# Kernel tuning notes

Hardware: AMD Instinct MI355X
Metric: run time of the kernel (lower is better)

The kernel has to match this reference:

```python
import jax, jax.numpy as jnp
import numpy as np

B, S, D = 2, 2048, 2048
NH, NKV = 16, 4
HD = D // NH          # 128
Q_DIM = NH * HD       # 2048
KV_DIM = NKV * HD     # 512
N_REP = NH // NKV     # 4


def setup_inputs() -> dict:
    key = jax.random.key(0)
    k1, k2, k3, k4 = jax.random.split(key, 4)
    x = jax.random.normal(k1, (B, S, D), dtype=jnp.float32)
    freqs_cis = jax.random.normal(k2, (S, HD), dtype=jnp.float32)
    Wqkv = jax.random.normal(k3, (Q_DIM + 2 * KV_DIM, D), dtype=jnp.float32) * (D ** -0.5)
    Wo = jax.random.normal(k4, (D, Q_DIM), dtype=jnp.float32) * (Q_DIM ** -0.5)
    return {"x": x, "freqs_cis": freqs_cis, "Wqkv": Wqkv, "Wo": Wo}


def _apply_rope(xq, xk, freqs_cis):
    # xq: [B,S,NH,HD], xk: [B,S,NKV,HD], freqs_cis: [S,HD] viewed as [S,1,HD//2,2]
    f = freqs_cis.reshape(S, 1, HD // 2, 2)
    f0, f1 = f[..., 0], f[..., 1]  # broadcast over batch & heads

    def rot(t):
        shp = t.shape
        tp = t.reshape(*shp[:-1], HD // 2, 2)
        t0, t1 = tp[..., 0], tp[..., 1]
        # row1 = <x, (f0,f1)>;  row0 = <x, (f1,-f0)>  (matches torch flip+negate)
        row1 = t0 * f0 + t1 * f1
        row0 = t0 * f1 - t1 * f0
        return jnp.stack([row0, row1], axis=-1).reshape(shp)

    return rot(xq), rot(xk)


def reference(x, freqs_cis, Wqkv, Wo):
    # Fused QKV projection (exact path: all RLA sketch dims = 0)
    xqkv = jnp.einsum('bsd,od->bso', x, Wqkv)
    xq = xqkv[..., :Q_DIM].reshape(B, S, NH, HD)
    xk = xqkv[..., Q_DIM:Q_DIM + KV_DIM].reshape(B, S, NKV, HD)
    xv = xqkv[..., Q_DIM + KV_DIM:].reshape(B, S, NKV, HD)

    xq, xk = _apply_rope(xq, xk, freqs_cis)

    # [B,H,S,HD]
    xq = xq.transpose(0, 2, 1, 3)
    xk = xk.transpose(0, 2, 1, 3)
    xv = xv.transpose(0, 2, 1, 3)

    # GQA: repeat kv heads n_rep times
    xk = jnp.repeat(xk, N_REP, axis=1)
    xv = jnp.repeat(xv, N_REP, axis=1)

    scale = 1.0 / jnp.sqrt(jnp.asarray(HD, dtype=xq.dtype))
    scores = jnp.einsum('bhqd,bhkd->bhqk', xq, xk) * scale
    causal = jnp.tril(jnp.ones((S, S), dtype=bool))
    scores = jnp.where(causal, scores, jnp.finfo(scores.dtype).min)
    probs = jax.nn.softmax(scores, axis=-1)
    out = jnp.einsum('bhqk,bhkd->bhqd', probs, xv)  # [B,H,S,HD]

    out = out.transpose(0, 2, 1, 3).reshape(B, S, Q_DIM)
    return jnp.einsum('bsq,dq->bsd', out, Wo)
```

## Files before the change

kernel.cpp:

```cpp
#include <hip/hip_runtime.h>
#include <hip/hip_bf16.h>
#include <cstdint>
#include <cstddef>

#define B_ 2
#define S_ 2048
#define NH_ 16
#define NKV_ 4
#define HD_ 128
#define QDIM_ 2048
#define KVDIM_ 512
#define QKV_ 3072

typedef __attribute__((ext_vector_type(8))) short short8;
typedef __attribute__((ext_vector_type(4))) short bhalf4;
typedef __attribute__((ext_vector_type(4))) float float4v;

__device__ __forceinline__ float bf2f(short u) {
  union { unsigned int i; float f; } v;
  v.i = ((unsigned int)(unsigned short)u) << 16;
  return v.f;
}
__device__ __forceinline__ short f2bf(float f) {
  union { float f; unsigned int i; } v; v.f = f;
  unsigned int x = v.i;
  x += 0x7fffu + ((x >> 16) & 1u);
  return (short)(x >> 16);
}

#if __has_builtin(__builtin_amdgcn_exp2f)
__device__ __forceinline__ float exp2fast(float x) { return __builtin_amdgcn_exp2f(x); }
#else
__device__ __forceinline__ float exp2fast(float x) { return exp2f(x); }
#endif

__device__ __forceinline__ unsigned int cvt_pk_bf16(float a, float b) {
  unsigned int r;
  asm("v_cvt_pk_bf16_f32 %0, %1, %2" : "=v"(r) : "v"(a), "v"(b));
  return r;
}

__device__ __forceinline__ void async_copy16(void* lds, const void* g) {
  __builtin_amdgcn_global_load_lds(
      (const __attribute__((address_space(1))) void*)g,
      (__attribute__((address_space(3))) void*)lds, 16, 0, 0);
}

__device__ __forceinline__ void cvt8(const float* f, short* d) {
  float4v a = *(const float4v*)(f);
  float4v b = *(const float4v*)(f + 4);
  short8 r;
#pragma unroll
  for (int e = 0; e < 4; ++e) { r[e] = f2bf(a[e]); r[4 + e] = f2bf(b[e]); }
  *(short8*)d = r;
}

__global__ void f32_to_bf16(const float* __restrict__ src, short* __restrict__ dst,
                            int n8) {
  int id = blockIdx.x * 256 + threadIdx.x;
  if (id >= n8) return;
  cvt8(src + (size_t)id * 8, dst + (size_t)id * 8);
}

__global__ void f32_to_bf16_2(const float* __restrict__ s0, short* __restrict__ d0,
                              int n0_8, const float* __restrict__ s1,
                              short* __restrict__ d1) {
  int id = blockIdx.x * 256 + threadIdx.x;
  if (id < n0_8) {
    cvt8(s0 + (size_t)id * 8, d0 + (size_t)id * 8);
  } else {
    int j = id - n0_8;
    cvt8(s1 + (size_t)j * 8, d1 + (size_t)j * 8);
  }
}

template <int N, int K, bool CF32>
__global__ __launch_bounds__(256)
void gemm_nt_bf16(const short* __restrict__ A, const short* __restrict__ Bm,
                  void* __restrict__ Cp) {
  __shared__ __align__(16) short sA[128 * 32];
  __shared__ __align__(16) short sB[128 * 32];
  const int tid = threadIdx.x;
  const int m0 = blockIdx.y * 128, n0 = blockIdx.x * 128;
  const int wave = tid >> 6, lane = tid & 63;
  const int wm = (wave & 1) << 6, wn = (wave >> 1) << 6;
  const int lm = lane & 15, kg = lane >> 4;

  float4v acc[4][4];
#pragma unroll
  for (int i = 0; i < 4; ++i)
#pragma unroll
    for (int j = 0; j < 4; ++j)
      acc[i][j] = (float4v){0.f, 0.f, 0.f, 0.f};

  const int r0 = tid >> 2, c0 = tid & 3;
  const short* gA0 = A + (size_t)(m0 + r0) * K + c0 * 8;
  const short* gA1 = gA0 + (size_t)64 * K;
  const short* gB0 = Bm + (size_t)(n0 + r0) * K + c0 * 8;
  const short* gB1 = gB0 + (size_t)64 * K;
  short* lA0 = sA + tid * 8;
  short* lA1 = sA + 2048 + tid * 8;
  short* lB0 = sB + tid * 8;
  short* lB1 = sB + 2048 + tid * 8;

  for (int k0 = 0; k0 < K; k0 += 32) {
    async_copy16(lA0, gA0 + k0);
    async_copy16(lA1, gA1 + k0);
    async_copy16(lB0, gB0 + k0);
    async_copy16(lB1, gB1 + k0);
    __syncthreads();

    short8 a[4], b[4];
#pragma unroll
    for (int i = 0; i < 4; ++i)
      a[i] = *(const short8*)(sA + (wm + i * 16 + lm) * 32 + kg * 8);
#pragma unroll
    for (int j = 0; j < 4; ++j)
      b[j] = *(const short8*)(sB + (wn + j * 16 + lm) * 32 + kg * 8);
#pragma unroll
    for (int i = 0; i < 4; ++i)
#pragma unroll
      for (int j = 0; j < 4; ++j)
        acc[i][j] = __builtin_amdgcn_mfma_f32_16x16x32_bf16(a[i], b[j], acc[i][j], 0, 0, 0);
    __syncthreads();
  }

#pragma unroll
  for (int i = 0; i < 4; ++i) {
    const int rb = m0 + wm + i * 16 + kg * 4;
#pragma unroll
    for (int j = 0; j < 4; ++j) {
      const int cc = n0 + wn + j * 16 + lm;
#pragma unroll
      for (int r = 0; r < 4; ++r) {
        if constexpr (CF32)
          ((float*)Cp)[(size_t)(rb + r) * N + cc] = acc[i][j][r];
        else
          ((short*)Cp)[(size_t)(rb + r) * N + cc] = f2bf(acc[i][j][r]);
      }
    }
  }
}

__global__ void rope_split(const short* __restrict__ xqkv, const float* __restrict__ freqs,
                           short* __restrict__ Qr, short* __restrict__ Kr,
                           short* __restrict__ Vv) {
  const int id = blockIdx.x * 256 + threadIdx.x;
  const int i = id / (QKV_ / 8);
  const int c8 = id % (QKV_ / 8);
  const int col = c8 * 8;
  const int b = i >> 11, s = i & (S_ - 1);
  short8 xv = *(const short8*)(xqkv + (size_t)i * QKV_ + col);
  if (col < QDIM_ + KVDIM_) {
    int d;
    short* dst;
    float sc;
    if (col < QDIM_) {
      int hh = col >> 7; d = col & 127;
      dst = Qr + ((size_t)(b * NH_ + hh) * S_ + s) * HD_ + d;
      sc = 0.12751744543795287f;
    } else {
      int cc = col - QDIM_;
      int hh = cc >> 7; d = cc & 127;
      dst = Kr + ((size_t)(b * NKV_ + hh) * S_ + s) * HD_ + d;
      sc = 1.0f;
    }
    const float* fp = freqs + (size_t)s * HD_ + d;
    float4v fa = *(const float4v*)(fp);
    float4v fb = *(const float4v*)(fp + 4);
    float ff[8] = {fa[0], fa[1], fa[2], fa[3], fb[0], fb[1], fb[2], fb[3]};
    short8 ov;
#pragma unroll
    for (int pp = 0; pp < 4; ++pp) {
      float t0 = bf2f(xv[2 * pp]), t1 = bf2f(xv[2 * pp + 1]);
      float f0 = ff[2 * pp], f1 = ff[2 * pp + 1];
      ov[2 * pp]     = f2bf((t0 * f1 - t1 * f0) * sc);
      ov[2 * pp + 1] = f2bf((t0 * f0 + t1 * f1) * sc);
    }
    *(short8*)dst = ov;
  } else {
    int cc = col - QDIM_ - KVDIM_;
    int hh = cc >> 7, d = cc & 127;
    *(short8*)(Vv + ((size_t)(b * NKV_ + hh) * S_ + s) * HD_ + d) = xv;
  }
}

__global__ void transpose_v(const short* __restrict__ Vv, short* __restrict__ Vt) {
  __shared__ short t[64][72];
  const int s0 = blockIdx.x * 64, d0 = blockIdx.y * 64;
  const short* src = Vv + (size_t)blockIdx.z * S_ * HD_;
  short* dst = Vt + (size_t)blockIdx.z * S_ * HD_;
  const int tid = threadIdx.x;
#pragma unroll
  for (int c = 0; c < 2; ++c) {
    int ch = tid + 256 * c;
    int row = ch >> 3, kc = ch & 7;
    *(short8*)(&t[row][kc * 8]) =
        *(const short8*)(src + (size_t)(s0 + row) * HD_ + d0 + kc * 8);
  }
  __syncthreads();
#pragma unroll
  for (int c = 0; c < 2; ++c) {
    int ch = tid + 256 * c;
    int drow = ch >> 3, sc = ch & 7;
    short8 w;
#pragma unroll
    for (int j = 0; j < 8; ++j) w[j] = t[sc * 8 + j][drow];
    *(short8*)(dst + (size_t)(d0 + drow) * S_ + s0 + sc * 8) = w;
  }
}

#define TK 128

__global__ __launch_bounds__(256, 2)
void attn_causal(const short* __restrict__ Q, const short* __restrict__ K,
                 const short* __restrict__ Vt, short* __restrict__ O) {
  const int bh = blockIdx.x;
  const int qt = 31 - (int)blockIdx.y;
  const int b = bh >> 4, h = bh & 15;
  const int kvh = h >> 2;
  const int tid = threadIdx.x, wave = tid >> 6, lane = tid & 63;
  const int lm = lane & 15, kg = lane >> 4;

  __shared__ __align__(16) short sK[TK * HD_];
  __shared__ __align__(16) short sVt[HD_ * TK];

  const short* Qb = Q + (size_t)(b * NH_ + h) * S_ * HD_;
  const short* Kb = K + (size_t)(b * NKV_ + kvh) * S_ * HD_;
  const short* Vtb = Vt + (size_t)(b * NKV_ + kvh) * S_ * HD_;

  auto stageK = [&](int k0) {
#pragma unroll
    for (int c = 0; c < 8; ++c) {
      int ch = tid + 256 * c;
      int row = ch >> 4, kc = ch & 15;
      async_copy16(sK + ch * 8,
                   Kb + (size_t)(k0 + row) * HD_ + (kc ^ (row & 7)) * 8);
    }
  };
  auto stageV = [&](int k0) {
#pragma unroll
    for (int c = 0; c < 8; ++c) {
      int ch = tid + 256 * c;
      int row = ch >> 4, kc = ch & 15;
      async_copy16(sVt + ch * 8,
                   Vtb + (size_t)row * S_ + k0 + (kc ^ (row & 7)) * 8);
    }
  };

  const int qglob = qt * 64 + wave * 16 + lm;
  short8 qf[4];
#pragma unroll
  for (int kk = 0; kk < 4; ++kk)
    qf[kk] = *(const short8*)(Qb + (size_t)qglob * HD_ + kk * 32 + kg * 8);

  float mcur = -1e9f, lcur = 0.f;
  float4v o[8];
#pragma unroll
  for (int df = 0; df < 8; ++df) o[df] = (float4v){0.f, 0.f, 0.f, 0.f};

  stageK(0);
  const int nst = (qt + 2) >> 1;
  for (int s = 0; s < nst; ++s) {
    const int k0 = s * TK;
    const bool last = (s == nst - 1);

    __syncthreads();
    stageV(k0);

    float4v sfT[8];
#pragma unroll
    for (int mj = 0; mj < 8; ++mj) sfT[mj] = (float4v){0.f, 0.f, 0.f, 0.f};
    __builtin_amdgcn_s_setprio(1);
#pragma unroll
    for (int kk = 0; kk < 4; ++kk) {
      int kd = kk * 4 + kg;
#pragma unroll
      for (int mj = 0; mj < 8; ++mj) {
        int row = mj * 16 + lm;
        short8 af = *(const short8*)(sK + row * HD_ + (kd ^ (row & 7)) * 8);
        sfT[mj] = __builtin_amdgcn_mfma_f32_16x16x32_bf16(af, qf[kk], sfT[mj], 0, 0, 0);
      }
    }
    __builtin_amdgcn_s_setprio(0);

    if (last) {
#pragma unroll
      for (int mj = 0; mj < 8; ++mj)
#pragma unroll
        for (int r = 0; r < 4; ++r) {
          int kcol = k0 + mj * 16 + kg * 4 + r;
          sfT[mj][r] = (kcol <= qglob) ? sfT[mj][r] : -3e38f;
        }
    }

    float mx = -3e38f;
#pragma unroll
    for (int mj = 0; mj < 8; ++mj)
#pragma unroll
      for (int r = 0; r < 4; ++r) mx = fmaxf(mx, sfT[mj][r]);
    mx = fmaxf(mx, __shfl_xor(mx, 16, 64));
    mx = fmaxf(mx, __shfl_xor(mx, 32, 64));
    const bool need = (mx > mcur + 4.f);
    const float mnew = fmaxf(mcur, mx);
    const float alpha = need ? exp2fast(mcur - mnew) : 1.f;
    const float m_use = need ? mnew : mcur;
    float rs = 0.f;
    bhalf4 pb[8];
#pragma unroll
    for (int t = 0; t < 8; ++t) {
      float e0 = exp2fast(sfT[t][0] - m_use);
      float e1 = exp2fast(sfT[t][1] - m_use);
      float e2 = exp2fast(sfT[t][2] - m_use);
      float e3 = exp2fast(sfT[t][3] - m_use);
      rs += (e0 + e1) + (e2 + e3);
      union { unsigned int u[2]; bhalf4 v; } pk;
      pk.u[0] = cvt_pk_bf16(e0, e1);
      pk.u[1] = cvt_pk_bf16(e2, e3);
      pb[t] = pk.v;
    }
    rs += __shfl_xor(rs, 16, 64);
    rs += __shfl_xor(rs, 32, 64);
    mcur = m_use;
    lcur = lcur * alpha + rs;

    __syncthreads();
    if (!last) stageK(k0 + TK);

    if (__any(need)) {
#pragma unroll
      for (int df = 0; df < 8; ++df)
#pragma unroll
        for (int r = 0; r < 4; ++r) o[df][r] *= alpha;
    }

    __builtin_amdgcn_s_setprio(1);
#pragma unroll
    for (int t = 0; t < 8; ++t) {
      int kc = t * 2 + (kg >> 1);
#pragma unroll
      for (int df = 0; df < 8; ++df) {
        int row = df * 16 + lm;
        bhalf4 va = *(const bhalf4*)(sVt + row * TK + (kc ^ (row & 7)) * 8 +
                                     (kg & 1) * 4);
        o[df] = __builtin_amdgcn_mfma_f32_16x16x16bf16_1k(va, pb[t], o[df], 0, 0, 0);
      }
    }
    __builtin_amdgcn_s_setprio(0);
  }

  const float inv = 1.f / lcur;
  const size_t rowoff = (size_t)(b * S_ + qglob) * QDIM_ + h * HD_ + kg * 4;
#pragma unroll
  for (int df = 0; df < 8; ++df) {
    bhalf4 w;
    w[0] = f2bf(o[df][0] * inv);
    w[1] = f2bf(o[df][1] * inv);
    w[2] = f2bf(o[df][2] * inv);
    w[3] = f2bf(o[df][3] * inv);
    *(bhalf4*)(O + rowoff + df * 16) = w;
  }
}

extern "C" void kernel_launch(void* const* d_in, const int* in_sizes, int n_in,
                              void* d_out, int out_size, void* d_ws, size_t ws_size,
                              hipStream_t stream) {
  const float* x     = (const float*)d_in[0];
  const float* freqs = (const float*)d_in[1];
  const float* Wqkv  = (const float*)d_in[2];
  const float* Wo    = (const float*)d_in[3];
  float* out = (float*)d_out;

  short* ws     = (short*)d_ws;
  short* xb     = ws;
  short* Wob    = ws;
  short* Wqkvb  = ws + (size_t)4096 * 2048;
  short* xqkv   = Wqkvb + (size_t)QKV_ * 2048;
  short* attn   = xqkv;
  short* Qr     = xqkv + (size_t)4096 * QKV_;
  short* Kr     = Qr + (size_t)B_ * NH_ * S_ * HD_;
  short* Vv     = Kr + (size_t)B_ * NKV_ * S_ * HD_;
  short* Vtg    = Vv + (size_t)B_ * NKV_ * S_ * HD_;

  f32_to_bf16_2<<<(4096 * 2048 / 8 + QKV_ * 2048 / 8) / 256, 256, 0, stream>>>(
      x, xb, 4096 * 2048 / 8, Wqkv, Wqkvb);
  gemm_nt_bf16<QKV_, 2048, false>
      <<<dim3(QKV_ / 128, 4096 / 128), 256, 0, stream>>>(xb, Wqkvb, xqkv);
  f32_to_bf16<<<(2048 * 2048 / 8) / 256, 256, 0, stream>>>(Wo, Wob, 2048 * 2048 / 8);
  rope_split<<<(B_ * S_ * QKV_ / 8) / 256, 256, 0, stream>>>(xqkv, freqs, Qr, Kr, Vv);
  transpose_v<<<dim3(S_ / 64, HD_ / 64, B_ * NKV_), 256, 0, stream>>>(Vv, Vtg);
  attn_causal<<<dim3(32, 32), 256, 0, stream>>>(Qr, Kr, Vtg, attn);
  gemm_nt_bf16<2048, 2048, true>
      <<<dim3(2048 / 128, 4096 / 128), 256, 0, stream>>>(attn, Wob, out);
}
```

Baseline: 309.6 us.

## Process 128 query rows per attention block to reuse K/V tiles

```diff
diff --git a/kernel.cpp b/kernel.cpp
--- a/kernel.cpp
+++ b/kernel.cpp
@@ -216,7 +216,8 @@
 void attn_causal(const short* __restrict__ Q, const short* __restrict__ K,
                  const short* __restrict__ Vt, short* __restrict__ O) {
   const int bh = blockIdx.x;
-  const int qt = 31 - (int)blockIdx.y;
+  const int by = blockIdx.y;
+  const int qt = (by < 8) ? (15 - by) : (by - 8);
   const int b = bh >> 4, h = bh & 15;
   const int kvh = h >> 2;
   const int tid = threadIdx.x, wave = tid >> 6, lane = tid & 63;
@@ -248,19 +249,24 @@
     }
   };
 
-  const int qglob = qt * 64 + wave * 16 + lm;
-  short8 qf[4];
-#pragma unroll
-  for (int kk = 0; kk < 4; ++kk)
-    qf[kk] = *(const short8*)(Qb + (size_t)qglob * HD_ + kk * 32 + kg * 8);
-
-  float mcur = -1e9f, lcur = 0.f;
-  float4v o[8];
-#pragma unroll
-  for (int df = 0; df < 8; ++df) o[df] = (float4v){0.f, 0.f, 0.f, 0.f};
+  const int qbase = qt * 128 + wave * 32 + lm;
+  short8 qf[2][4];
+#pragma unroll
+  for (int u = 0; u < 2; ++u)
+#pragma unroll
+    for (int kk = 0; kk < 4; ++kk)
+      qf[u][kk] = *(const short8*)(Qb + (size_t)(qbase + u * 16) * HD_ +
+                                   kk * 32 + kg * 8);
+
+  float mcur[2] = {-1e9f, -1e9f}, lcur[2] = {0.f, 0.f};
+  float4v o[2][8];
+#pragma unroll
+  for (int u = 0; u < 2; ++u)
+#pragma unroll
+    for (int df = 0; df < 8; ++df) o[u][df] = (float4v){0.f, 0.f, 0.f, 0.f};
 
   stageK(0);
-  const int nst = (qt + 2) >> 1;
+  const int nst = qt + 1;
   for (int s = 0; s < nst; ++s) {
     const int k0 = s * TK;
     const bool last = (s == nst - 1);
@@ -268,9 +274,11 @@
     __syncthreads();
     stageV(k0);
 
-    float4v sfT[8];
-#pragma unroll
-    for (int mj = 0; mj < 8; ++mj) sfT[mj] = (float4v){0.f, 0.f, 0.f, 0.f};
+    float4v sf[2][8];
+#pragma unroll
+    for (int u = 0; u < 2; ++u)
+#pragma unroll
+      for (int mj = 0; mj < 8; ++mj) sf[u][mj] = (float4v){0.f, 0.f, 0.f, 0.f};
     __builtin_amdgcn_s_setprio(1);
 #pragma unroll
     for (int kk = 0; kk < 4; ++kk) {
@@ -279,59 +287,72 @@
       for (int mj = 0; mj < 8; ++mj) {
         int row = mj * 16 + lm;
         short8 af = *(const short8*)(sK + row * HD_ + (kd ^ (row & 7)) * 8);
-        sfT[mj] = __builtin_amdgcn_mfma_f32_16x16x32_bf16(af, qf[kk], sfT[mj], 0, 0, 0);
+        sf[0][mj] = __builtin_amdgcn_mfma_f32_16x16x32_bf16(af, qf[0][kk], sf[0][mj], 0, 0, 0);
+        sf[1][mj] = __builtin_amdgcn_mfma_f32_16x16x32_bf16(af, qf[1][kk], sf[1][mj], 0, 0, 0);
       }
     }
     __builtin_amdgcn_s_setprio(0);
 
     if (last) {
 #pragma unroll
+      for (int u = 0; u < 2; ++u) {
+        const int qg = qbase + u * 16;
+#pragma unroll
+        for (int mj = 0; mj < 8; ++mj)
+#pragma unroll
+          for (int r = 0; r < 4; ++r) {
+            int kcol = k0 + mj * 16 + kg * 4 + r;
+            sf[u][mj][r] = (kcol <= qg) ? sf[u][mj][r] : -3e38f;
+          }
+      }
+    }
+
+    bhalf4 pb[2][8];
+    bool need[2];
+    float alpha[2];
+#pragma unroll
+    for (int u = 0; u < 2; ++u) {
+      float mx = -3e38f;
+#pragma unroll
       for (int mj = 0; mj < 8; ++mj)
 #pragma unroll
-        for (int r = 0; r < 4; ++r) {
-          int kcol = k0 + mj * 16 + kg * 4 + r;
-          sfT[mj][r] = (kcol <= qglob) ? sfT[mj][r] : -3e38f;
-        }
-    }
-
-    float mx = -3e38f;
-#pragma unroll
-    for (int mj = 0; mj < 8; ++mj)
-#pragma unroll
-      for (int r = 0; r < 4; ++r) mx = fmaxf(mx, sfT[mj][r]);
-    mx = fmaxf(mx, __shfl_xor(mx, 16, 64));
-    mx = fmaxf(mx, __shfl_xor(mx, 32, 64));
-    const bool need = (mx > mcur + 4.f);
-    const float mnew = fmaxf(mcur, mx);
-    const float alpha = need ? exp2fast(mcur - mnew) : 1.f;
-    const float m_use = need ? mnew : mcur;
-    float rs = 0.f;
-    bhalf4 pb[8];
-#pragma unroll
-    for (int t = 0; t < 8; ++t) {
-      float e0 = exp2fast(sfT[t][0] - m_use);
-      float e1 = exp2fast(sfT[t][1] - m_use);
-      float e2 = exp2fast(sfT[t][2] - m_use);
-      float e3 = exp2fast(sfT[t][3] - m_use);
-      rs += (e0 + e1) + (e2 + e3);
-      union { unsigned int u[2]; bhalf4 v; } pk;
-      pk.u[0] = cvt_pk_bf16(e0, e1);
-      pk.u[1] = cvt_pk_bf16(e2, e3);
-      pb[t] = pk.v;
-    }
-    rs += __shfl_xor(rs, 16, 64);
-    rs += __shfl_xor(rs, 32, 64);
-    mcur = m_use;
-    lcur = lcur * alpha + rs;
+        for (int r = 0; r < 4; ++r) mx = fmaxf(mx, sf[u][mj][r]);
+      mx = fmaxf(mx, __shfl_xor(mx, 16, 64));
+      mx = fmaxf(mx, __shfl_xor(mx, 32, 64));
+      need[u] = (mx > mcur[u] + 4.f);
+      const float mnew = fmaxf(mcur[u], mx);
+      alpha[u] = need[u] ? exp2fast(mcur[u] - mnew) : 1.f;
+      const float m_use = need[u] ? mnew : mcur[u];
+      float rs = 0.f;
+#pragma unroll
+      for (int t = 0; t < 8; ++t) {
+        float e0 = exp2fast(sf[u][t][0] - m_use);
+        float e1 = exp2fast(sf[u][t][1] - m_use);
+        float e2 = exp2fast(sf[u][t][2] - m_use);
+        float e3 = exp2fast(sf[u][t][3] - m_use);
+        rs += (e0 + e1) + (e2 + e3);
+        union { unsigned int w[2]; bhalf4 v; } pk;
+        pk.w[0] = cvt_pk_bf16(e0, e1);
+        pk.w[1] = cvt_pk_bf16(e2, e3);
+        pb[u][t] = pk.v;
+      }
+      rs += __shfl_xor(rs, 16, 64);
+      rs += __shfl_xor(rs, 32, 64);
+      mcur[u] = m_use;
+      lcur[u] = lcur[u] * alpha[u] + rs;
+    }
 
     __syncthreads();
     if (!last) stageK(k0 + TK);
 
-    if (__any(need)) {
-#pragma unroll
-      for (int df = 0; df < 8; ++df)
-#pragma unroll
-        for (int r = 0; r < 4; ++r) o[df][r] *= alpha;
+#pragma unroll
+    for (int u = 0; u < 2; ++u) {
+      if (__any(need[u])) {
+#pragma unroll
+        for (int df = 0; df < 8; ++df)
+#pragma unroll
+          for (int r = 0; r < 4; ++r) o[u][df][r] *= alpha[u];
+      }
     }
 
     __builtin_amdgcn_s_setprio(1);
@@ -343,22 +364,27 @@
         int row = df * 16 + lm;
         bhalf4 va = *(const bhalf4*)(sVt + row * TK + (kc ^ (row & 7)) * 8 +
                                      (kg & 1) * 4);
-        o[df] = __builtin_amdgcn_mfma_f32_16x16x16bf16_1k(va, pb[t], o[df], 0, 0, 0);
+        o[0][df] = __builtin_amdgcn_mfma_f32_16x16x16bf16_1k(va, pb[0][t], o[0][df], 0, 0, 0);
+        o[1][df] = __builtin_amdgcn_mfma_f32_16x16x16bf16_1k(va, pb[1][t], o[1][df], 0, 0, 0);
       }
     }
     __builtin_amdgcn_s_setprio(0);
   }
 
-  const float inv = 1.f / lcur;
-  const size_t rowoff = (size_t)(b * S_ + qglob) * QDIM_ + h * HD_ + kg * 4;
-#pragma unroll
-  for (int df = 0; df < 8; ++df) {
-    bhalf4 w;
-    w[0] = f2bf(o[df][0] * inv);
-    w[1] = f2bf(o[df][1] * inv);
-    w[2] = f2bf(o[df][2] * inv);
-    w[3] = f2bf(o[df][3] * inv);
-    *(bhalf4*)(O + rowoff + df * 16) = w;
+#pragma unroll
+  for (int u = 0; u < 2; ++u) {
+    const float inv = 1.f / lcur[u];
+    const size_t rowoff =
+        (size_t)(b * S_ + qbase + u * 16) * QDIM_ + h * HD_ + kg * 4;
+#pragma unroll
+    for (int df = 0; df < 8; ++df) {
+      bhalf4 w;
+      w[0] = f2bf(o[u][df][0] * inv);
+      w[1] = f2bf(o[u][df][1] * inv);
+      w[2] = f2bf(o[u][df][2] * inv);
+      w[3] = f2bf(o[u][df][3] * inv);
+      *(bhalf4*)(O + rowoff + df * 16) = w;
+    }
   }
 }
 
@@ -389,7 +415,7 @@
   f32_to_bf16<<<(2048 * 2048 / 8) / 256, 256, 0, stream>>>(Wo, Wob, 2048 * 2048 / 8);
   rope_split<<<(B_ * S_ * QKV_ / 8) / 256, 256, 0, stream>>>(xqkv, freqs, Qr, Kr, Vv);
   transpose_v<<<dim3(S_ / 64, HD_ / 64, B_ * NKV_), 256, 0, stream>>>(Vv, Vtg);
-  attn_causal<<<dim3(32, 32), 256, 0, stream>>>(Qr, Kr, Vtg, attn);
+  attn_causal<<<dim3(32, 16), 256, 0, stream>>>(Qr, Kr, Vtg, attn);
   gemm_nt_bf16<2048, 2048, true>
       <<<dim3(2048 / 128, 4096 / 128), 256, 0, stream>>>(attn, Wob, out);
 }
```

Result: slower. 342.6 us (+10.7%).
